# Kernel tuning notes

Measured on AMD Instinct MI355X. Metric: run time of the kernel, lower is better.

## Reference

```python
import jax, jax.numpy as jnp
import numpy as np
jax.config.update("jax_enable_x64", True)  # hashing uses int64 primes as in torch

N_PTS = 1048576
L, T, F = 16, 2 ** 18, 2
N_MIN, N_MAX = 16, 1024
HID, OUT = 64, 3


def setup_inputs() -> dict:
    key = jax.random.key(0)
    ks = jax.random.split(key, 6)
    X = jax.random.uniform(ks[0], (N_PTS, 2), dtype=jnp.float32)
    hash_table = jax.random.uniform(ks[1], (L, T, F), dtype=jnp.float32,
                                    minval=-1e-4, maxval=1e-4)
    def lin(k, fan_in, fan_out):
        bound = 1.0 / np.sqrt(fan_in)
        kw, kb = jax.random.split(k)
        W = jax.random.uniform(kw, (fan_in, fan_out), dtype=jnp.float32,
                               minval=-bound, maxval=bound)
        b = jax.random.uniform(kb, (fan_out,), dtype=jnp.float32,
                               minval=-bound, maxval=bound)
        return W, b
    W1, b1 = lin(ks[2], L * F, HID)
    W2, b2 = lin(ks[3], HID, HID)
    W3, b3 = lin(ks[4], HID, HID)
    W4, b4 = lin(ks[5], HID, OUT)
    return {"X": X, "hash_table": hash_table,
            "W1": W1, "b1": b1, "W2": W2, "b2": b2,
            "W3": W3, "b3": b3, "W4": W4, "b4": b4}


def reference(X, hash_table, W1, b1, W2, b2, W3, b3, W4, b4):
    Lh, Th, Fh = hash_table.shape
    # per-level resolutions: floor(N_min * b**l), b geometric between N_min and N_max
    b_geo = np.exp((np.log(N_MAX) - np.log(N_MIN)) / (Lh - 1))
    N_values = jnp.floor(jnp.asarray(N_MIN * b_geo ** np.arange(Lh),
                                     dtype=jnp.float32))  # (L,)

    x_scaled = X[:, :, None] * N_values[None, None, :]        # (N, 2, L)
    x_floor = jnp.floor(x_scaled)

    # NOTE: original code MULTIPLIES floor coords by the 0/1 vertex pattern
    # (not add) -- we replicate that math faithfully.
    vertices = jnp.array([[0., 0., 1., 1.], [0., 1., 0., 1.]],
                         dtype=jnp.float32)                   # (2, 4)
    x_vert = (x_floor[:, :, :, None] * vertices[None, :, None, :]
              ).astype(jnp.int64)                             # (N, 2, L, 4)

    primes = jnp.array([1, 2654435761], dtype=jnp.int64)
    hv = x_vert * primes[None, :, None, None]
    x_hash = jnp.remainder(jnp.bitwise_xor(hv[:, 0], hv[:, 1]), Th)  # (N, L, 4)

    # irregular gather: per-level hash table lookup -> (N, L, 4, F)
    lookup = hash_table[jnp.arange(Lh)[None, :, None], x_hash]

    w = x_scaled - x_floor                                    # (N, 2, L)
    fx, fy = w[:, 0, :], w[:, 1, :]
    cx, cy = 1.0 - fx, 1.0 - fy
    f_stack = jnp.stack([cx * cy, cx * fy, fx * cy, fx * fy], axis=2)  # (N, L, 4)

    x_interp = jnp.sum(f_stack[:, :, :, None] * lookup, axis=2)  # (N, L, F)
    feat = x_interp.reshape(-1, Lh * Fh).astype(jnp.float32)     # (N, 32)

    h = jax.nn.leaky_relu(feat @ W1 + b1)
    h = jax.nn.leaky_relu(h @ W2 + b2)
    h = jax.nn.leaky_relu(h @ W3 + b3)
    return jax.nn.relu(h @ W4 + b4)
```

## Files before the change

kernel.cpp:

```cpp
#include <hip/hip_runtime.h>
#include <math.h>

typedef _Float16 half8  __attribute__((ext_vector_type(8)));
typedef float    float4v __attribute__((ext_vector_type(4)));

constexpr int T_ = 1 << 18;
constexpr unsigned TMASK = T_ - 1;
constexpr unsigned PRIME = 2654435761u;
constexpr int HP = 72;

constexpr int WFRAG_HALFS = 22 * 64 * 8;
constexpr int BIAS_FLOATS = 208;
constexpr int WS_BYTES    = 22528 + 240 * 4;
constexpr int WS_UINT4    = WS_BYTES / 16;
constexpr int MAX_STAGE   = 4224;

constexpr int BLK   = 512;
constexpr int WAVES = 8;
constexpr int PTS_PER_BLOCK = 1024;

struct Meta { float n[16]; float off[16]; };

__global__ void prep_weights(const float* __restrict__ W1, const float* __restrict__ b1,
                             const float* __restrict__ W2, const float* __restrict__ b2,
                             const float* __restrict__ W3, const float* __restrict__ b3,
                             const float* __restrict__ W4, const float* __restrict__ b4,
                             _Float16* __restrict__ wsW, float* __restrict__ wsB, Meta mv)
{
    const int tid = threadIdx.x;
    if (blockIdx.x < 44) {
        const int e = blockIdx.x * 256 + tid;
        const int frag = e >> 9;
        const int l    = (e >> 3) & 63;
        const int j    = e & 7;
        const int g = l >> 4, m = l & 15;
        float v;
        if (frag < 4) {
            v = W1[(8*g + j) * 64 + 16*frag + m];
        } else if (frag < 12) {
            const int s = (frag - 4) >> 2, t = (frag - 4) & 3;
            v = W2[(32*s + 8*g + j) * 64 + 16*t + m];
        } else if (frag < 20) {
            const int s = (frag - 12) >> 2, t = (frag - 12) & 3;
            v = W3[(32*s + 8*g + j) * 64 + 16*t + m];
        } else {
            const int s = frag - 20;
            v = (m < 3) ? W4[(32*s + 8*g + j) * 3 + m] : 0.f;
        }
        wsW[e] = (_Float16)v;
    } else {
        if (tid < 64) { wsB[tid] = b1[tid]; wsB[64 + tid] = b2[tid]; wsB[128 + tid] = b3[tid]; }
        else if (tid < 80)  { const int r = tid - 64; wsB[192 + r] = (r < 3) ? b4[r] : 0.f; }
        else if (tid < 96)  wsB[BIAS_FLOATS + (tid - 80)] = mv.n[tid - 80];
        else if (tid < 112) wsB[BIAS_FLOATS + 16 + (tid - 96)] = mv.off[tid - 96];
    }
}

#define DS_FENCE() __asm__ volatile("s_waitcnt lgkmcnt(0)" ::: "memory")

struct Gather {
    float  fx[4], fy[4];
    float2 v1[4], v2[4], v3[4];
};

__device__ __forceinline__ void issue_gather(Gather& G, const float2 xy,
                                             const float2* __restrict__ table,
                                             const float (&nvq)[4], const int (&offq)[4],
                                             const float2* __restrict__ sV1,
                                             const float2* __restrict__ sV2, const int g)
{
    #pragma unroll
    for (int q = 0; q < 4; ++q) {
        const int lv = 4*g + q;
        const float n = nvq[q];
        const float xs = xy.x * n, ys = xy.y * n;
        const float xf = floorf(xs), yf = floorf(ys);
        G.fx[q] = xs - xf; G.fy[q] = ys - yf;
        const unsigned xi = (unsigned)(int)xf, yi = (unsigned)(int)yf;
        const unsigned yp = yi * PRIME;
        G.v3[q] = table[(size_t)lv * T_ + ((xi ^ yp) & TMASK)];
        G.v1[q] = sV1[offq[q] + (int)yi];
        G.v2[q] = sV2[offq[q] + (int)xi];
    }
}

__device__ __forceinline__ half8 combine_feat(const Gather& G, const float2 (&v0c)[4])
{
    half8 feat;
    #pragma unroll
    for (int q = 0; q < 4; ++q) {
        const float fx = G.fx[q], fy = G.fy[q];
        const float cx = 1.f - fx, cy = 1.f - fy;
        const float w0 = cx*cy, w1 = cx*fy, w2 = fx*cy, w3 = fx*fy;
        feat[2*q+0] = (_Float16)(w0*v0c[q].x + w1*G.v1[q].x + w2*G.v2[q].x + w3*G.v3[q].x);
        feat[2*q+1] = (_Float16)(w0*v0c[q].y + w1*G.v1[q].y + w2*G.v2[q].y + w3*G.v3[q].y);
    }
    return feat;
}

__global__ __launch_bounds__(BLK)
void fused_hashnerf_mfma(const float2* __restrict__ X,
                         const float2* __restrict__ table,
                         const uint4* __restrict__ ws,
                         float* __restrict__ out)
{
    __shared__ uint4    sRaw[WS_UINT4];
    __shared__ _Float16 sH[WAVES][16 * HP];
    __shared__ float2   sV1[MAX_STAGE];
    __shared__ float2   sV2[MAX_STAGE];

    const int tid = threadIdx.x;
    for (int i = tid; i < WS_UINT4; i += BLK) sRaw[i] = ws[i];
    __syncthreads();

    const _Float16* Wl = (const _Float16*)sRaw;
    const float*    Bl = (const float*)(sRaw + (22528 / 16));

    {
        const float* NVp = Bl + BIAS_FLOATS;
        const float* OFp = Bl + BIAS_FLOATS + 16;
        for (int l = 0; l < 16; ++l) {
            const int nl  = (int)NVp[l];
            const int off = (int)OFp[l];
            const float2* tl = table + (size_t)l * T_;
            for (int i = tid; i <= nl; i += BLK) {
                sV2[off + i] = tl[i];
                sV1[off + i] = tl[((unsigned)i * PRIME) & TMASK];
            }
        }
    }
    __syncthreads();

    const int wave = tid >> 6, lane = tid & 63;
    const int g = lane >> 4, c = lane & 15;
    _Float16* H = &sH[wave][0];

    float4v b1f[4], b2f[4], b3f[4], b4f;
    #pragma unroll
    for (int t = 0; t < 4; ++t) {
        b1f[t] = *(const float4v*)(Bl +       16*t + 4*g);
        b2f[t] = *(const float4v*)(Bl +  64 + 16*t + 4*g);
        b3f[t] = *(const float4v*)(Bl + 128 + 16*t + 4*g);
    }
    b4f = *(const float4v*)(Bl + 192 + 4*g);
    float nvq[4];
    int   offq[4];
    #pragma unroll
    for (int q = 0; q < 4; ++q) {
        nvq[q]  = Bl[BIAS_FLOATS + 4*g + q];
        offq[q] = (int)Bl[BIAS_FLOATS + 16 + 4*g + q];
    }

    const int base_pt = blockIdx.x * PTS_PER_BLOCK + wave * 128;

    float2 xy[8];
    #pragma unroll
    for (int it = 0; it < 8; ++it) xy[it] = X[base_pt + it*16 + c];

    float2 v0c[4];
    #pragma unroll
    for (int q = 0; q < 4; ++q) v0c[q] = table[(size_t)(4*g + q) * T_];

    Gather GA, GB;
    issue_gather(GA, xy[0], table, nvq, offq, sV1, sV2, g);

    #pragma unroll
    for (int it = 0; it < 8; ++it) {
        Gather& Gc = (it & 1) ? GB : GA;
        Gather& Gn = (it & 1) ? GA : GB;

        const half8 feat = combine_feat(Gc, v0c);

        if (it < 7) issue_gather(Gn, xy[it+1], table, nvq, offq, sV1, sV2, g);
        __builtin_amdgcn_sched_barrier(0);

        float4v acc[4];
        #pragma unroll
        for (int t = 0; t < 4; ++t) {
            const half8 wf = *(const half8*)(Wl + (t*64 + lane)*8);
            acc[t] = __builtin_amdgcn_mfma_f32_16x16x32_f16(wf, feat, b1f[t], 0, 0, 0);
        }
        #pragma unroll
        for (int t = 0; t < 4; ++t) {
            union { _Float16 h[4]; float2 f2; } u;
            #pragma unroll
            for (int r = 0; r < 4; ++r) {
                const float v = acc[t][r];
                u.h[r] = (_Float16)(v > 0.f ? v : 0.01f * v);
            }
            *(float2*)(H + c*HP + 16*t + 4*g) = u.f2;
        }
        DS_FENCE();

        half8 a0 = *(const half8*)(H + c*HP +      8*g);
        half8 a1 = *(const half8*)(H + c*HP + 32 + 8*g);
        float4v acc2[4];
        #pragma unroll
        for (int t = 0; t < 4; ++t) {
            const half8 w0f = *(const half8*)(Wl + ((4 + t)*64 + lane)*8);
            const half8 w1f = *(const half8*)(Wl + ((8 + t)*64 + lane)*8);
            float4v a = __builtin_amdgcn_mfma_f32_16x16x32_f16(w0f, a0, b2f[t], 0, 0, 0);
            acc2[t]   = __builtin_amdgcn_mfma_f32_16x16x32_f16(w1f, a1, a,      0, 0, 0);
        }
        #pragma unroll
        for (int t = 0; t < 4; ++t) {
            union { _Float16 h[4]; float2 f2; } u;
            #pragma unroll
            for (int r = 0; r < 4; ++r) {
                const float v = acc2[t][r];
                u.h[r] = (_Float16)(v > 0.f ? v : 0.01f * v);
            }
            *(float2*)(H + c*HP + 16*t + 4*g) = u.f2;
        }
        DS_FENCE();

        a0 = *(const half8*)(H + c*HP +      8*g);
        a1 = *(const half8*)(H + c*HP + 32 + 8*g);
        float4v acc3[4];
        #pragma unroll
        for (int t = 0; t < 4; ++t) {
            const half8 w0f = *(const half8*)(Wl + ((12 + t)*64 + lane)*8);
            const half8 w1f = *(const half8*)(Wl + ((16 + t)*64 + lane)*8);
            float4v a = __builtin_amdgcn_mfma_f32_16x16x32_f16(w0f, a0, b3f[t], 0, 0, 0);
            acc3[t]   = __builtin_amdgcn_mfma_f32_16x16x32_f16(w1f, a1, a,      0, 0, 0);
        }
        #pragma unroll
        for (int t = 0; t < 4; ++t) {
            union { _Float16 h[4]; float2 f2; } u;
            #pragma unroll
            for (int r = 0; r < 4; ++r) {
                const float v = acc3[t][r];
                u.h[r] = (_Float16)(v > 0.f ? v : 0.01f * v);
            }
            *(float2*)(H + c*HP + 16*t + 4*g) = u.f2;
        }
        DS_FENCE();

        a0 = *(const half8*)(H + c*HP +      8*g);
        a1 = *(const half8*)(H + c*HP + 32 + 8*g);
        const half8 w40 = *(const half8*)(Wl + (20*64 + lane)*8);
        const half8 w41 = *(const half8*)(Wl + (21*64 + lane)*8);
        float4v o = __builtin_amdgcn_mfma_f32_16x16x32_f16(w40, a0, b4f, 0, 0, 0);
        o         = __builtin_amdgcn_mfma_f32_16x16x32_f16(w41, a1, o,   0, 0, 0);
        if (g == 0) {
            const int p = base_pt + it * 16 + c;
            float* op = out + (size_t)3 * p;
            op[0] = fmaxf(o[0], 0.f);
            op[1] = fmaxf(o[1], 0.f);
            op[2] = fmaxf(o[2], 0.f);
        }
    }
}

extern "C" void kernel_launch(void* const* d_in, const int* in_sizes, int n_in,
                              void* d_out, int out_size, void* d_ws, size_t ws_size,
                              hipStream_t stream) {
    const float2* X     = (const float2*)d_in[0];
    const float2* table = (const float2*)d_in[1];
    const float*  W1    = (const float*)d_in[2];
    const float*  b1    = (const float*)d_in[3];
    const float*  W2    = (const float*)d_in[4];
    const float*  b2    = (const float*)d_in[5];
    const float*  W3    = (const float*)d_in[6];
    const float*  b3    = (const float*)d_in[7];
    const float*  W4    = (const float*)d_in[8];
    const float*  b4    = (const float*)d_in[9];
    float* out          = (float*)d_out;

    const int npts = in_sizes[0] / 2;

    Meta mv;
    const double bg = exp((log(1024.0) - log(16.0)) / 15.0);
    int acc = 0;
    for (int l = 0; l < 16; ++l) {
        const float nl = floorf((float)(16.0 * pow(bg, (double)l)));
        mv.n[l]   = nl;
        mv.off[l] = (float)acc;
        acc += (int)nl + 1;
    }

    _Float16* wsW = (_Float16*)d_ws;
    float*    wsB = (float*)((char*)d_ws + 22528);

    prep_weights<<<45, 256, 0, stream>>>(W1, b1, W2, b2, W3, b3, W4, b4, wsW, wsB, mv);
    fused_hashnerf_mfma<<<npts / PTS_PER_BLOCK, BLK, 0, stream>>>(X, table, (const uint4*)d_ws, out);
}
```

Measured before the change: 220.1 us.

## Process two point tiles per iteration and prefetch only hashed corner

The per-wave loop now handles two 16-point tiles per iteration. Their independent MFMA chains are interleaved, and each tile gets its own LDS activation buffer, so MFMA latency and LDS round-trips can overlap. The software prefetch now covers only the global hashed-corner gather, two tiles ahead, while the LDS-staged corners and fractional weights are recomputed at combine time, which lowers live register state. The cost is doubled sH shared memory and more accumulator registers, which could reduce occupancy.

```diff
diff --git a/kernel.cpp b/kernel.cpp
--- a/kernel.cpp
+++ b/kernel.cpp
@@ -58,44 +58,56 @@
 
 #define DS_FENCE() __asm__ volatile("s_waitcnt lgkmcnt(0)" ::: "memory")
 
-struct Gather {
-    float  fx[4], fy[4];
-    float2 v1[4], v2[4], v3[4];
-};
-
-__device__ __forceinline__ void issue_gather(Gather& G, const float2 xy,
-                                             const float2* __restrict__ table,
-                                             const float (&nvq)[4], const int (&offq)[4],
-                                             const float2* __restrict__ sV1,
-                                             const float2* __restrict__ sV2, const int g)
+struct V3Pair { float2 a[4]; float2 b[4]; };
+
+__device__ __forceinline__ void issue_v3(float2 (&v3)[4], const float2 xy,
+                                         const float2* __restrict__ table,
+                                         const float (&nvq)[4], const int g)
 {
     #pragma unroll
     for (int q = 0; q < 4; ++q) {
-        const int lv = 4*g + q;
+        const float n = nvq[q];
+        const float xs = xy.x * n, ys = xy.y * n;
+        const unsigned xi = (unsigned)(int)floorf(xs);
+        const unsigned yi = (unsigned)(int)floorf(ys);
+        v3[q] = table[(size_t)(4*g + q) * T_ + ((xi ^ (yi * PRIME)) & TMASK)];
+    }
+}
+
+__device__ __forceinline__ half8 make_feat(const float2 xy, const float2 (&v3)[4],
+                                           const float (&nvq)[4], const int (&offq)[4],
+                                           const float2* __restrict__ sV1,
+                                           const float2* __restrict__ sV2,
+                                           const float2 (&v0c)[4])
+{
+    half8 feat;
+    #pragma unroll
+    for (int q = 0; q < 4; ++q) {
         const float n = nvq[q];
         const float xs = xy.x * n, ys = xy.y * n;
         const float xf = floorf(xs), yf = floorf(ys);
-        G.fx[q] = xs - xf; G.fy[q] = ys - yf;
-        const unsigned xi = (unsigned)(int)xf, yi = (unsigned)(int)yf;
-        const unsigned yp = yi * PRIME;
-        G.v3[q] = table[(size_t)lv * T_ + ((xi ^ yp) & TMASK)];
-        G.v1[q] = sV1[offq[q] + (int)yi];
-        G.v2[q] = sV2[offq[q] + (int)xi];
-    }
-}
-
-__device__ __forceinline__ half8 combine_feat(const Gather& G, const float2 (&v0c)[4])
-{
-    half8 feat;
-    #pragma unroll
-    for (int q = 0; q < 4; ++q) {
-        const float fx = G.fx[q], fy = G.fy[q];
+        const float fx = xs - xf, fy = ys - yf;
+        const int xi = (int)xf, yi = (int)yf;
+        const float2 v1 = sV1[offq[q] + yi];
+        const float2 v2 = sV2[offq[q] + xi];
         const float cx = 1.f - fx, cy = 1.f - fy;
         const float w0 = cx*cy, w1 = cx*fy, w2 = fx*cy, w3 = fx*fy;
-        feat[2*q+0] = (_Float16)(w0*v0c[q].x + w1*G.v1[q].x + w2*G.v2[q].x + w3*G.v3[q].x);
-        feat[2*q+1] = (_Float16)(w0*v0c[q].y + w1*G.v1[q].y + w2*G.v2[q].y + w3*G.v3[q].y);
+        feat[2*q+0] = (_Float16)(w0*v0c[q].x + w1*v1.x + w2*v2.x + w3*v3[q].x);
+        feat[2*q+1] = (_Float16)(w0*v0c[q].y + w1*v1.y + w2*v2.y + w3*v3[q].y);
     }
     return feat;
+}
+
+__device__ __forceinline__ void act_store(_Float16* __restrict__ H, const int c,
+                                          const int g, const int t, const float4v acc)
+{
+    union { _Float16 h[4]; float2 f2; } u;
+    #pragma unroll
+    for (int r = 0; r < 4; ++r) {
+        const float v = acc[r];
+        u.h[r] = (_Float16)(v > 0.f ? v : 0.01f * v);
+    }
+    *(float2*)(H + c*HP + 16*t + 4*g) = u.f2;
 }
 
 __global__ __launch_bounds__(BLK)
@@ -105,7 +117,7 @@
                          float* __restrict__ out)
 {
     __shared__ uint4    sRaw[WS_UINT4];
-    __shared__ _Float16 sH[WAVES][16 * HP];
+    __shared__ _Float16 sH[WAVES * 2][16 * HP];
     __shared__ float2   sV1[MAX_STAGE];
     __shared__ float2   sV2[MAX_STAGE];
 
@@ -133,7 +145,8 @@
 
     const int wave = tid >> 6, lane = tid & 63;
     const int g = lane >> 4, c = lane & 15;
-    _Float16* H = &sH[wave][0];
+    _Float16* Ha = &sH[2*wave + 0][0];
+    _Float16* Hb = &sH[2*wave + 1][0];
 
     float4v b1f[4], b2f[4], b3f[4], b4f;
     #pragma unroll
@@ -161,93 +174,84 @@
     #pragma unroll
     for (int q = 0; q < 4; ++q) v0c[q] = table[(size_t)(4*g + q) * T_];
 
-    Gather GA, GB;
-    issue_gather(GA, xy[0], table, nvq, offq, sV1, sV2, g);
-
-    #pragma unroll
-    for (int it = 0; it < 8; ++it) {
-        Gather& Gc = (it & 1) ? GB : GA;
-        Gather& Gn = (it & 1) ? GA : GB;
-
-        const half8 feat = combine_feat(Gc, v0c);
-
-        if (it < 7) issue_gather(Gn, xy[it+1], table, nvq, offq, sV1, sV2, g);
+    V3Pair PA, PB;
+    issue_v3(PA.a, xy[0], table, nvq, g);
+    issue_v3(PA.b, xy[1], table, nvq, g);
+
+    #pragma unroll
+    for (int p = 0; p < 4; ++p) {
+        V3Pair& Pc = (p & 1) ? PB : PA;
+        V3Pair& Pn = (p & 1) ? PA : PB;
+
+        const half8 fa = make_feat(xy[2*p+0], Pc.a, nvq, offq, sV1, sV2, v0c);
+        const half8 fb = make_feat(xy[2*p+1], Pc.b, nvq, offq, sV1, sV2, v0c);
+
+        if (p < 3) {
+            issue_v3(Pn.a, xy[2*p+2], table, nvq, g);
+            issue_v3(Pn.b, xy[2*p+3], table, nvq, g);
+        }
         __builtin_amdgcn_sched_barrier(0);
 
-        float4v acc[4];
+        float4v aA[4], aB[4];
         #pragma unroll
         for (int t = 0; t < 4; ++t) {
             const half8 wf = *(const half8*)(Wl + (t*64 + lane)*8);
-            acc[t] = __builtin_amdgcn_mfma_f32_16x16x32_f16(wf, feat, b1f[t], 0, 0, 0);
-        }
-        #pragma unroll
-        for (int t = 0; t < 4; ++t) {
-            union { _Float16 h[4]; float2 f2; } u;
-            #pragma unroll
-            for (int r = 0; r < 4; ++r) {
-                const float v = acc[t][r];
-                u.h[r] = (_Float16)(v > 0.f ? v : 0.01f * v);
-            }
-            *(float2*)(H + c*HP + 16*t + 4*g) = u.f2;
-        }
+            aA[t] = __builtin_amdgcn_mfma_f32_16x16x32_f16(wf, fa, b1f[t], 0, 0, 0);
+            aB[t] = __builtin_amdgcn_mfma_f32_16x16x32_f16(wf, fb, b1f[t], 0, 0, 0);
+        }
+        #pragma unroll
+        for (int t = 0; t < 4; ++t) { act_store(Ha, c, g, t, aA[t]); act_store(Hb, c, g, t, aB[t]); }
         DS_FENCE();
 
-        half8 a0 = *(const half8*)(H + c*HP +      8*g);
-        half8 a1 = *(const half8*)(H + c*HP + 32 + 8*g);
-        float4v acc2[4];
+        half8 a0A = *(const half8*)(Ha + c*HP +      8*g);
+        half8 a1A = *(const half8*)(Ha + c*HP + 32 + 8*g);
+        half8 a0B = *(const half8*)(Hb + c*HP +      8*g);
+        half8 a1B = *(const half8*)(Hb + c*HP + 32 + 8*g);
         #pragma unroll
         for (int t = 0; t < 4; ++t) {
             const half8 w0f = *(const half8*)(Wl + ((4 + t)*64 + lane)*8);
             const half8 w1f = *(const half8*)(Wl + ((8 + t)*64 + lane)*8);
-            float4v a = __builtin_amdgcn_mfma_f32_16x16x32_f16(w0f, a0, b2f[t], 0, 0, 0);
-            acc2[t]   = __builtin_amdgcn_mfma_f32_16x16x32_f16(w1f, a1, a,      0, 0, 0);
-        }
-        #pragma unroll
-        for (int t = 0; t < 4; ++t) {
-            union { _Float16 h[4]; float2 f2; } u;
-            #pragma unroll
-            for (int r = 0; r < 4; ++r) {
-                const float v = acc2[t][r];
-                u.h[r] = (_Float16)(v > 0.f ? v : 0.01f * v);
-            }
-            *(float2*)(H + c*HP + 16*t + 4*g) = u.f2;
-        }
+            float4v xA = __builtin_amdgcn_mfma_f32_16x16x32_f16(w0f, a0A, b2f[t], 0, 0, 0);
+            float4v xB = __builtin_amdgcn_mfma_f32_16x16x32_f16(w0f, a0B, b2f[t], 0, 0, 0);
+            aA[t] = __builtin_amdgcn_mfma_f32_16x16x32_f16(w1f, a1A, xA, 0, 0, 0);
+            aB[t] = __builtin_amdgcn_mfma_f32_16x16x32_f16(w1f, a1B, xB, 0, 0, 0);
+        }
+        #pragma unroll
+        for (int t = 0; t < 4; ++t) { act_store(Ha, c, g, t, aA[t]); act_store(Hb, c, g, t, aB[t]); }
         DS_FENCE();
 
-        a0 = *(const half8*)(H + c*HP +      8*g);
-        a1 = *(const half8*)(H + c*HP + 32 + 8*g);
-        float4v acc3[4];
+        a0A = *(const half8*)(Ha + c*HP +      8*g);
+        a1A = *(const half8*)(Ha + c*HP + 32 + 8*g);
+        a0B = *(const half8*)(Hb + c*HP +      8*g);
+        a1B = *(const half8*)(Hb + c*HP + 32 + 8*g);
         #pragma unroll
         for (int t = 0; t < 4; ++t) {
             const half8 w0f = *(const half8*)(Wl + ((12 + t)*64 + lane)*8);
             const half8 w1f = *(const half8*)(Wl + ((16 + t)*64 + lane)*8);
-            float4v a = __builtin_amdgcn_mfma_f32_16x16x32_f16(w0f, a0, b3f[t], 0, 0, 0);
-            acc3[t]   = __builtin_amdgcn_mfma_f32_16x16x32_f16(w1f, a1, a,      0, 0, 0);
-        }
-        #pragma unroll
-        for (int t = 0; t < 4; ++t) {
-            union { _Float16 h[4]; float2 f2; } u;
-            #pragma unroll
-            for (int r = 0; r < 4; ++r) {
-                const float v = acc3[t][r];
-                u.h[r] = (_Float16)(v > 0.f ? v : 0.01f * v);
-            }
-            *(float2*)(H + c*HP + 16*t + 4*g) = u.f2;
-        }
+            float4v xA = __builtin_amdgcn_mfma_f32_16x16x32_f16(w0f, a0A, b3f[t], 0, 0, 0);
+            float4v xB = __builtin_amdgcn_mfma_f32_16x16x32_f16(w0f, a0B, b3f[t], 0, 0, 0);
+            aA[t] = __builtin_amdgcn_mfma_f32_16x16x32_f16(w1f, a1A, xA, 0, 0, 0);
+            aB[t] = __builtin_amdgcn_mfma_f32_16x16x32_f16(w1f, a1B, xB, 0, 0, 0);
+        }
+        #pragma unroll
+        for (int t = 0; t < 4; ++t) { act_store(Ha, c, g, t, aA[t]); act_store(Hb, c, g, t, aB[t]); }
         DS_FENCE();
 
-        a0 = *(const half8*)(H + c*HP +      8*g);
-        a1 = *(const half8*)(H + c*HP + 32 + 8*g);
+        a0A = *(const half8*)(Ha + c*HP +      8*g);
+        a1A = *(const half8*)(Ha + c*HP + 32 + 8*g);
+        a0B = *(const half8*)(Hb + c*HP +      8*g);
+        a1B = *(const half8*)(Hb + c*HP + 32 + 8*g);
         const half8 w40 = *(const half8*)(Wl + (20*64 + lane)*8);
         const half8 w41 = *(const half8*)(Wl + (21*64 + lane)*8);
-        float4v o = __builtin_amdgcn_mfma_f32_16x16x32_f16(w40, a0, b4f, 0, 0, 0);
-        o         = __builtin_amdgcn_mfma_f32_16x16x32_f16(w41, a1, o,   0, 0, 0);
+        float4v oA = __builtin_amdgcn_mfma_f32_16x16x32_f16(w40, a0A, b4f, 0, 0, 0);
+        float4v oB = __builtin_amdgcn_mfma_f32_16x16x32_f16(w40, a0B, b4f, 0, 0, 0);
+        oA = __builtin_amdgcn_mfma_f32_16x16x32_f16(w41, a1A, oA, 0, 0, 0);
+        oB = __builtin_amdgcn_mfma_f32_16x16x32_f16(w41, a1B, oB, 0, 0, 0);
         if (g == 0) {
-            const int p = base_pt + it * 16 + c;
-            float* op = out + (size_t)3 * p;
-            op[0] = fmaxf(o[0], 0.f);
-            op[1] = fmaxf(o[1], 0.f);
-            op[2] = fmaxf(o[2], 0.f);
+            float* opA = out + (size_t)3 * (base_pt + (2*p+0)*16 + c);
+            float* opB = out + (size_t)3 * (base_pt + (2*p+1)*16 + c);
+            opA[0] = fmaxf(oA[0], 0.f); opA[1] = fmaxf(oA[1], 0.f); opA[2] = fmaxf(oA[2], 0.f);
+            opB[0] = fmaxf(oB[0], 0.f); opB[1] = fmaxf(oB[1], 0.f); opB[2] = fmaxf(oB[2], 0.f);
         }
     }
 }
```

Result: slower. 227.1 us (+3.1%).
